# Kernel optimization log

Measured on AMD Instinct MI355X. Metric: run time of the kernel, lower is better.

## Reference

```python
import jax, jax.numpy as jnp
import numpy as np

# Dims (match init_kwargs): d_model=1024, H=16 heads, hd=64, lift=2 -> Nlift=128, top-k t=32
B, T, D = 1, 2048, 1024
H, HD, LIFT, TK = 16, 64, 2, 32
N = LIFT * HD  # 128 lifted dims per head
EPS = 1e-12


def topk_sparsify(x, k):
    """ReLU then keep only the top-k values per last-dim row (rest zeroed).
    Mathematically identical to the torch COO top-k construction: the sparse
    matrix equals the dense matrix with non-top-k entries zeroed."""
    x = jax.nn.relu(x)
    vals, idx = jax.lax.top_k(x, k)              # (..., k)
    n = x.shape[-1]
    flat_idx = idx.reshape(-1, k)
    flat_vals = vals.reshape(-1, k)
    R = flat_idx.shape[0]
    out = jnp.zeros((R, n), dtype=x.dtype)
    out = out.at[jnp.arange(R)[:, None], flat_idx].set(flat_vals)
    return out.reshape(x.shape)


def setup_inputs() -> dict:
    key = jax.random.key(0)
    ks = jax.random.split(key, 6)
    x = jax.random.normal(ks[0], (B, T, D), jnp.float32)
    W_q = jax.random.normal(ks[1], (H * N, D), jnp.float32) * 0.02
    W_k = jax.random.normal(ks[2], (H * N, D), jnp.float32) * 0.02
    W_v = jax.random.normal(ks[3], (H * HD, D), jnp.float32) * 0.02
    W_o = jax.random.normal(ks[4], (D, H * HD), jnp.float32) * 0.02
    sink = jax.random.normal(ks[5], (H, HD), jnp.float32) * 0.02
    log_beta = jnp.zeros((), jnp.float32)
    return {"x": x, "W_q": W_q, "W_k": W_k, "W_v": W_v, "W_o": W_o,
            "sink": sink, "log_beta": log_beta}


def reference(x, W_q, W_k, W_v, W_o, sink, log_beta):
    # Projections (Linear with no bias: x @ W.T)
    q = (x @ W_q.T).reshape(B, T, H, N)
    k = (x @ W_k.T).reshape(B, T, H, N)
    v = (x @ W_v.T).reshape(B, T, H, HD)

    # ReLU + top-k sparsification of lifted Q/K rows
    qs = topk_sparsify(q, TK).transpose(0, 2, 1, 3)  # (B,H,T,N)
    kk = topk_sparsify(k, TK).transpose(0, 2, 1, 3)  # (B,H,T,N)

    # A = Qs @ Ks^T per (batch, head) block; spspmm only produces same-block
    # entries, so the per-head batched matmul is the exact dense equivalent.
    A = jnp.einsum('bhin,bhjn->bhij', qs, kk)        # (B,H,T,T), all >= 0

    # Causal filter: keep j <= i
    causal = jnp.tril(jnp.ones((T, T), dtype=bool))
    A = jnp.where(causal, A, jnp.zeros((), A.dtype))

    # p=1 normalization with learned sink mass beta
    denom = A.sum(-1)                                # (B,H,T)
    beta = jnp.exp(log_beta)
    denom_ws = denom + beta
    A = A / jnp.maximum(denom_ws, EPS)[..., None]

    vh = v.transpose(0, 2, 1, 3)                     # (B,H,T,HD)
    Y = jnp.einsum('bhij,bhjd->bhid', A, vh)         # (B,H,T,HD)
    Y = Y + (beta / denom_ws)[..., None] * sink[None, :, None, :]

    Y = Y.transpose(0, 2, 1, 3).reshape(B, T, H * HD)
    return Y @ W_o.T
```

## Files before the change

### kernel.cpp

```cpp
#include <hip/hip_runtime.h>

typedef __attribute__((ext_vector_type(8))) short bf8v;
typedef __attribute__((ext_vector_type(4))) float f4v;
typedef unsigned short u16;
typedef unsigned int   u32;
#define AS1 __attribute__((address_space(1)))
#define AS3 __attribute__((address_space(3)))

__device__ inline u16 f2b(float f){
  u32 u = __builtin_bit_cast(u32, f);
  u += 0x7fffu + ((u >> 16) & 1u);
  return (u16)(u >> 16);
}

__global__ __launch_bounds__(256) void conv_all(const float* __restrict__ x,  const float* __restrict__ wq,
                                                const float* __restrict__ wk, const float* __restrict__ wv,
                                                const float* __restrict__ wo,
                                                u16* xb, u16* wqb, u16* wkb, u16* wvb, u16* wob){
  int i = blockIdx.x * 256 + threadIdx.x;
  const float* src; u16* dst; int off;
  if      (i <  524288){ src = x;  dst = xb;  off = i; }
  else if (i < 1048576){ src = wq; dst = wqb; off = i -  524288; }
  else if (i < 1572864){ src = wk; dst = wkb; off = i - 1048576; }
  else if (i < 1835008){ src = wv; dst = wvb; off = i - 1572864; }
  else                 { src = wo; dst = wob; off = i - 1835008; }
  float4 v = ((const float4*)src)[off];
  uint2 r;
  r.x = (u32)f2b(v.x) | ((u32)f2b(v.y) << 16);
  r.y = (u32)f2b(v.z) | ((u32)f2b(v.w) << 16);
  ((uint2*)dst)[off] = r;
}

template<int NFR>
__device__ __forceinline__ void gemm_core(const u16* __restrict__ A, const u16* __restrict__ B,
                                          int K, int m0, int n0, u16* lds, f4v (&acc)[4][NFR]){
  const int tid = threadIdx.x;
  const int l = tid & 63, w = tid >> 6;
  const int wrow = (w >> 1) * 64, wcol = (w & 1) * (NFR * 16);
  constexpr int SB = 8192 + NFR * 2048;
  #pragma unroll
  for (int a = 0; a < 4; a++)
    #pragma unroll
    for (int b = 0; b < NFR; b++) acc[a][b] = (f4v)0.0f;

  const int crow = l >> 3;
  const int ksrc = ((l & 7) ^ crow) * 8;

  auto stage = [&](int k0, int buf){
    const u16* Ab = A + (size_t)m0 * K + k0;
    const u16* Bb = B + (size_t)n0 * K + k0;
    u16* At = lds + buf * SB;
    u16* Bt = At + 8192;
    #pragma unroll
    for (int c = 0; c < 4; c++){
      int chunk = w * 4 + c;
      int row = chunk * 8 + crow;
      __builtin_amdgcn_global_load_lds((const AS1 void*)(Ab + (size_t)row * K + ksrc),
                                       (AS3 void*)(At + chunk * 512), 16, 0, 0);
    }
    if constexpr (NFR == 4){
      #pragma unroll
      for (int c = 0; c < 4; c++){
        int chunk = w * 4 + c;
        int row = chunk * 8 + crow;
        __builtin_amdgcn_global_load_lds((const AS1 void*)(Bb + (size_t)row * K + ksrc),
                                         (AS3 void*)(Bt + chunk * 512), 16, 0, 0);
      }
    } else {
      #pragma unroll
      for (int c = 0; c < 2; c++){
        int chunk = w * 2 + c;
        int row = chunk * 8 + crow;
        __builtin_amdgcn_global_load_lds((const AS1 void*)(Bb + (size_t)row * K + ksrc),
                                         (AS3 void*)(Bt + chunk * 512), 16, 0, 0);
      }
    }
  };

  stage(0, 0);
  __syncthreads();
  int buf = 0;
  for (int k0 = 0; k0 < K; k0 += 64){
    if (k0 + 64 < K) stage(k0 + 64, buf ^ 1);
    const u16* At = lds + buf * SB;
    const u16* Bt = At + 8192;
    #pragma unroll
    for (int kk = 0; kk < 2; kk++){
      bf8v af[4], bfr[NFR];
      #pragma unroll
      for (int mr = 0; mr < 4; mr++){
        int row = wrow + mr * 16 + (l & 15);
        af[mr] = *(const bf8v*)(At + row * 64 + (((kk * 32 + (l >> 4) * 8)) ^ ((row & 7) * 8)));
      }
      #pragma unroll
      for (int nc = 0; nc < NFR; nc++){
        int row = wcol + nc * 16 + (l & 15);
        bfr[nc] = *(const bf8v*)(Bt + row * 64 + (((kk * 32 + (l >> 4) * 8)) ^ ((row & 7) * 8)));
      }
      #pragma unroll
      for (int mr = 0; mr < 4; mr++)
        #pragma unroll
        for (int nc = 0; nc < NFR; nc++)
          acc[mr][nc] = __builtin_amdgcn_mfma_f32_16x16x32_bf16(af[mr], bfr[nc], acc[mr][nc], 0, 0, 0);
    }
    __syncthreads();
    buf ^= 1;
  }
}

__global__ __launch_bounds__(256) void qkv_gemm(const u16* __restrict__ xb,
                                                const u16* __restrict__ wqb, const u16* __restrict__ wkb,
                                                const u16* __restrict__ wvb,
                                                u16* qsb, u16* ksb, u16* vtb){
  __shared__ u16 lds[32768];
  int b = (blockIdx.x & 7) * 80 + (blockIdx.x >> 3);
  const u16* Bp; int which;
  if (b < 256)      { Bp = wqb; which = 0; }
  else if (b < 512) { Bp = wkb; which = 1; b -= 256; }
  else              { Bp = wvb; which = 2; b -= 512; }
  int sh = (which == 2) ? 3 : 4;
  int m0 = (b >> sh) * 128, n0 = (b & ((1 << sh) - 1)) * 128;

  f4v acc[4][4];
  gemm_core<4>(xb, Bp, 1024, m0, n0, lds, acc);

  const int l = threadIdx.x & 63, w = threadIdx.x >> 6;
  const int wrow = (w >> 1) * 64, wcol = (w & 1) * 64;
  if (which < 2){
    u16* Sc = lds;
    #pragma unroll
    for (int mr = 0; mr < 4; mr++)
      #pragma unroll
      for (int nc = 0; nc < 4; nc++)
        #pragma unroll
        for (int rr = 0; rr < 4; rr++){
          int row = wrow + mr * 16 + (l >> 4) * 4 + rr;
          int col = wcol + nc * 16 + (l & 15);
          float v = acc[mr][nc][rr];
          Sc[row * 132 + col] = (v > 0.f) ? f2b(v) : (u16)0;
        }
    __syncthreads();
    u16* dst = which ? ksb : qsb;
    const int h = n0 >> 7;
    for (int r2 = 0; r2 < 32; ++r2){
      int r = w * 32 + r2;
      u32 pair = *(const u32*)(Sc + r * 132 + l * 2);
      u32 u0 = pair & 0xFFFFu, u1 = pair >> 16;
      u32 pre = 0;
      for (int bb = 14; bb >= 0; --bb){
        u32 cand = pre | (1u << bb);
        int c = __builtin_popcountll(__ballot(u0 >= cand)) + __builtin_popcountll(__ballot(u1 >= cand));
        if (c >= 32) pre = cand;
      }
      u32 o0 = (u0 >= pre) ? u0 : 0u;
      u32 o1 = (u1 >= pre) ? u1 : 0u;
      ((u32*)(dst + ((size_t)h * 2048 + m0 + r) * 128))[l] = o0 | (o1 << 16);
    }
  } else {
    #pragma unroll
    for (int mr = 0; mr < 4; mr++)
      #pragma unroll
      for (int nc = 0; nc < 4; nc++){
        int gcol = n0 + wcol + nc * 16 + (l & 15);
        int t0 = m0 + wrow + mr * 16 + (l >> 4) * 4;
        uint2 pk;
        pk.x = (u32)f2b(acc[mr][nc][0]) | ((u32)f2b(acc[mr][nc][1]) << 16);
        pk.y = (u32)f2b(acc[mr][nc][2]) | ((u32)f2b(acc[mr][nc][3]) << 16);
        *(uint2*)(vtb + (size_t)gcol * 2048 + t0) = pk;
      }
  }
}

__global__ __launch_bounds__(256) void o_gemm(const u16* __restrict__ yb, const u16* __restrict__ wob,
                                              float* out){
  __shared__ u16 lds[24576];
  int b = (blockIdx.x & 7) * 32 + (blockIdx.x >> 3);
  int m0 = (b >> 4) * 128, n0 = (b & 15) * 64;
  f4v acc[4][2];
  gemm_core<2>(yb, wob, 1024, m0, n0, lds, acc);
  const int l = threadIdx.x & 63, w = threadIdx.x >> 6;
  const int wrow = (w >> 1) * 64, wcol = (w & 1) * 32;
  #pragma unroll
  for (int mr = 0; mr < 4; mr++)
    #pragma unroll
    for (int nc = 0; nc < 2; nc++)
      #pragma unroll
      for (int rr = 0; rr < 4; rr++){
        int row = m0 + wrow + mr * 16 + (l >> 4) * 4 + rr;
        int col = n0 + wcol + nc * 16 + (l & 15);
        out[(size_t)row * 1024 + col] = acc[mr][nc][rr];
      }
}

__global__ __launch_bounds__(512) void attn3(const u16* __restrict__ qs, const u16* __restrict__ ks,
                                             const u16* __restrict__ vt, const float* __restrict__ sink,
                                             const float* __restrict__ logbeta, u16* __restrict__ yout,
                                             float* __restrict__ Yp, float* __restrict__ Dp){
  __shared__ u16 Kt[2][8192];
  __shared__ u16 Vt[2][4096];
  __shared__ u16 St[8][16 * 72];
  const int tid = threadIdx.x, l = tid & 63, w = tid >> 6;
  const int b = blockIdx.x;
  const int slot = b >> 3;
  const int h = (b & 7) + 8 * (slot / 40);
  const int u = slot % 40;
  int it, chunk, nch;
  if (u < 4)       { it = u; chunk = 0; nch = 1; }
  else if (u < 12) { it = 4 + ((u - 4) >> 1);  chunk = (u - 4) & 1;  nch = 2; }
  else if (u < 24) { it = 8 + (u - 12) / 3;    chunk = (u - 12) % 3; nch = 3; }
  else             { it = 12 + ((u - 24) >> 2); chunk = (u - 24) & 3; nch = 4; }
  const int tiles = 2 * it + 2;
  const int jt0 = (tiles * chunk) / nch;
  const int jt1 = (tiles * (chunk + 1)) / nch;
  const int qrow0 = it * 128 + w * 16;
  const float beta = expf(logbeta[0]);

  bf8v qfr[4];
  {
    int trow = qrow0 + (l & 15);
    const u16* qrow = qs + ((size_t)h * 2048 + trow) * 128 + (l >> 4) * 8;
    #pragma unroll
    for (int kk = 0; kk < 4; kk++) qfr[kk] = *(const bf8v*)(qrow + kk * 32);
  }

  f4v accY[4];
  #pragma unroll
  for (int c = 0; c < 4; c++) accY[c] = (f4v)0.0f;
  float dsum[4] = {0.f, 0.f, 0.f, 0.f};

  const u16* kroot = ks + (size_t)h * 2048 * 128;
  const u16* vroot = vt + (size_t)h * 64 * 2048;

  auto stage = [&](int jt, int buf){
    const u16* kbase = kroot + (size_t)jt * 64 * 128;
    #pragma unroll
    for (int i = 0; i < 2; i++){
      int g = i * 512 + tid;
      int r = g >> 4, c = g & 15;
      __builtin_amdgcn_global_load_lds((const AS1 void*)(kbase + r * 128 + (c ^ (r & 7)) * 8),
                                       (AS3 void*)(&Kt[buf][(i * 512 + w * 64) * 8]), 16, 0, 0);
    }
    {
      int d = tid >> 3, c = tid & 7;
      __builtin_amdgcn_global_load_lds((const AS1 void*)(vroot + (size_t)d * 2048 + jt * 64 + (c ^ (d & 7)) * 8),
                                       (AS3 void*)(&Vt[buf][w * 512]), 16, 0, 0);
    }
  };

  stage(jt0, 0);
  __syncthreads();
  int buf = 0;
  for (int jt = jt0; jt < jt1; ++jt){
    if (jt + 1 < jt1) stage(jt + 1, buf ^ 1);

    if (jt * 64 <= qrow0 + 15){
      f4v accS[4];
      #pragma unroll
      for (int c = 0; c < 4; c++) accS[c] = (f4v)0.0f;
      __builtin_amdgcn_s_setprio(1);
      #pragma unroll
      for (int c = 0; c < 4; c++){
        int r = c * 16 + (l & 15);
        #pragma unroll
        for (int kk = 0; kk < 4; kk++){
          int ch = kk * 4 + (l >> 4);
          bf8v kfr = *(const bf8v*)(&Kt[buf][r * 128 + ((ch ^ (r & 7)) * 8)]);
          accS[c] = __builtin_amdgcn_mfma_f32_16x16x32_bf16(qfr[kk], kfr, accS[c], 0, 0, 0);
        }
      }
      __builtin_amdgcn_s_setprio(0);
      if (jt * 64 + 63 > qrow0){
        #pragma unroll
        for (int c = 0; c < 4; c++)
          #pragma unroll
          for (int rr = 0; rr < 4; rr++){
            int i = qrow0 + (l >> 4) * 4 + rr;
            int j = jt * 64 + c * 16 + (l & 15);
            if (j > i) accS[c][rr] = 0.f;
          }
      }
      #pragma unroll
      for (int c = 0; c < 4; c++)
        #pragma unroll
        for (int rr = 0; rr < 4; rr++){
          dsum[rr] += accS[c][rr];
          St[w][((l >> 4) * 4 + rr) * 72 + c * 16 + (l & 15)] = f2b(accS[c][rr]);
        }
      __builtin_amdgcn_s_setprio(1);
      #pragma unroll
      for (int k2 = 0; k2 < 2; k2++){
        bf8v afr = *(const bf8v*)(&St[w][(l & 15) * 72 + k2 * 32 + (l >> 4) * 8]);
        #pragma unroll
        for (int c = 0; c < 4; c++){
          int d = c * 16 + (l & 15);
          int ch = k2 * 4 + (l >> 4);
          bf8v vfr = *(const bf8v*)(&Vt[buf][d * 64 + ((ch ^ (d & 7)) * 8)]);
          accY[c] = __builtin_amdgcn_mfma_f32_16x16x32_bf16(afr, vfr, accY[c], 0, 0, 0);
        }
      }
      __builtin_amdgcn_s_setprio(0);
    }
    __syncthreads();
    buf ^= 1;
  }

  #pragma unroll
  for (int rr = 0; rr < 4; rr++){
    float s = dsum[rr];
    s += __shfl_xor(s, 1, 64);
    s += __shfl_xor(s, 2, 64);
    s += __shfl_xor(s, 4, 64);
    s += __shfl_xor(s, 8, 64);
    dsum[rr] = s;
  }

  if (nch == 1){
    #pragma unroll
    for (int c = 0; c < 4; c++){
      float sv = sink[h * 64 + c * 16 + (l & 15)];
      #pragma unroll
      for (int rr = 0; rr < 4; rr++){
        float den = dsum[rr] + beta;
        float inv = 1.0f / fmaxf(den, 1e-12f);
        float y = (accY[c][rr] + beta * sv) * inv;
        int row = qrow0 + (l >> 4) * 4 + rr;
        yout[(size_t)row * 1024 + h * 64 + c * 16 + (l & 15)] = f2b(y);
      }
    }
  } else {
    float* yp = Yp + ((size_t)h * 40 + u) * 8192;
    #pragma unroll
    for (int c = 0; c < 4; c++)
      #pragma unroll
      for (int rr = 0; rr < 4; rr++){
        int rowib = w * 16 + (l >> 4) * 4 + rr;
        yp[rowib * 64 + c * 16 + (l & 15)] = accY[c][rr];
      }
    if ((l & 15) == 0){
      #pragma unroll
      for (int rr = 0; rr < 4; rr++)
        Dp[((size_t)h * 40 + u) * 128 + w * 16 + (l >> 4) * 4 + rr] = dsum[rr];
    }
  }
}

__global__ __launch_bounds__(256) void attn_reduce(const float* __restrict__ Yp, const float* __restrict__ Dp,
                                                   const float* __restrict__ sink, const float* __restrict__ logbeta,
                                                   u16* __restrict__ yout){
  int blk = blockIdx.x;
  int h = blk / 12, it = 4 + blk % 12;
  int nch = it / 4 + 1;
  int u0 = (it < 8) ? 4 + (it - 4) * 2 : (it < 12) ? 12 + (it - 8) * 3 : 24 + (it - 12) * 4;
  float beta = expf(logbeta[0]);
  __shared__ float inv_s[128];
  int t = threadIdx.x;
  if (t < 128){
    float s = 0.f;
    for (int c = 0; c < nch; c++) s += Dp[((size_t)h * 40 + u0 + c) * 128 + t];
    inv_s[t] = 1.0f / fmaxf(s + beta, 1e-12f);
  }
  __syncthreads();
  const float* base = Yp + ((size_t)h * 40 + u0) * 8192;
  #pragma unroll
  for (int e = 0; e < 32; e++){
    int idx = e * 256 + t;
    float acc = 0.f;
    for (int c = 0; c < nch; c++) acc += base[c * 8192 + idx];
    int row = idx >> 6, col = idx & 63;
    float y = (acc + beta * sink[h * 64 + col]) * inv_s[row];
    yout[(size_t)(it * 128 + row) * 1024 + h * 64 + col] = f2b(y);
  }
}

extern "C" void kernel_launch(void* const* d_in, const int* in_sizes, int n_in,
                              void* d_out, int out_size, void* d_ws, size_t ws_size,
                              hipStream_t stream){
  const float* x    = (const float*)d_in[0];
  const float* Wq   = (const float*)d_in[1];
  const float* Wk   = (const float*)d_in[2];
  const float* Wv   = (const float*)d_in[3];
  const float* Wo   = (const float*)d_in[4];
  const float* sink = (const float*)d_in[5];
  const float* logb = (const float*)d_in[6];

  char* ws = (char*)d_ws;
  u16*   xb  = (u16*)(ws + 0);
  u16*   wqb = (u16*)(ws + 4194304);
  u16*   wkb = (u16*)(ws + 8388608);
  u16*   wvb = (u16*)(ws + 12582912);
  u16*   wob = (u16*)(ws + 14680064);
  float* Yp  = (float*)(ws + 16777216);
  float* Dp  = (float*)(ws + 37748736);
  u16*   qsb = (u16*)(ws + 50331648);
  u16*   ksb = (u16*)(ws + 58720256);
  u16*   vtb = (u16*)(ws + 67108864);
  u16*   yb  = (u16*)(ws + 71303168);

  conv_all<<<8192, 256, 0, stream>>>(x, Wq, Wk, Wv, Wo, xb, wqb, wkb, wvb, wob);
  qkv_gemm<<<640, 256, 0, stream>>>(xb, wqb, wkb, wvb, qsb, ksb, vtb);
  attn3<<<640, 512, 0, stream>>>(qsb, ksb, vtb, sink, logb, yb, Yp, Dp);
  attn_reduce<<<192, 256, 0, stream>>>(Yp, Dp, sink, logb, yb);
  o_gemm<<<256, 256, 0, stream>>>(yb, wob, (float*)d_out);
}
```

Measured before the change: 149.6 us.

## Split top-k sparsification out of QKV GEMM epilogue into separate kernel

The QKV GEMM now writes raw bf16 Q/K projections to a workspace buffer. A new topk2 kernel then applies ReLU and the bitwise threshold search for the top-32 per row, handling four rows per wave so the serial ballot loop gains instruction-level parallelism. This removes the long serial epilogue from the GEMM blocks, but it adds a kernel launch and an extra global write and read of the full Q/K tensors. The workspace region used for the partial Y buffers is reused for these intermediates.

```diff
diff --git a/kernel.cpp b/kernel.cpp
--- a/kernel.cpp
+++ b/kernel.cpp
@@ -111,7 +111,7 @@
 __global__ __launch_bounds__(256) void qkv_gemm(const u16* __restrict__ xb,
                                                 const u16* __restrict__ wqb, const u16* __restrict__ wkb,
                                                 const u16* __restrict__ wvb,
-                                                u16* qsb, u16* ksb, u16* vtb){
+                                                u16* qf, u16* kf, u16* vtb){
   __shared__ u16 lds[32768];
   int b = (blockIdx.x & 7) * 80 + (blockIdx.x >> 3);
   const u16* Bp; int which;
@@ -127,35 +127,17 @@
   const int l = threadIdx.x & 63, w = threadIdx.x >> 6;
   const int wrow = (w >> 1) * 64, wcol = (w & 1) * 64;
   if (which < 2){
-    u16* Sc = lds;
+    u16* C = which ? kf : qf;
     #pragma unroll
     for (int mr = 0; mr < 4; mr++)
       #pragma unroll
       for (int nc = 0; nc < 4; nc++)
         #pragma unroll
         for (int rr = 0; rr < 4; rr++){
-          int row = wrow + mr * 16 + (l >> 4) * 4 + rr;
-          int col = wcol + nc * 16 + (l & 15);
-          float v = acc[mr][nc][rr];
-          Sc[row * 132 + col] = (v > 0.f) ? f2b(v) : (u16)0;
+          int row = m0 + wrow + mr * 16 + (l >> 4) * 4 + rr;
+          int col = n0 + wcol + nc * 16 + (l & 15);
+          C[(size_t)row * 2048 + col] = f2b(acc[mr][nc][rr]);
         }
-    __syncthreads();
-    u16* dst = which ? ksb : qsb;
-    const int h = n0 >> 7;
-    for (int r2 = 0; r2 < 32; ++r2){
-      int r = w * 32 + r2;
-      u32 pair = *(const u32*)(Sc + r * 132 + l * 2);
-      u32 u0 = pair & 0xFFFFu, u1 = pair >> 16;
-      u32 pre = 0;
-      for (int bb = 14; bb >= 0; --bb){
-        u32 cand = pre | (1u << bb);
-        int c = __builtin_popcountll(__ballot(u0 >= cand)) + __builtin_popcountll(__ballot(u1 >= cand));
-        if (c >= 32) pre = cand;
-      }
-      u32 o0 = (u0 >= pre) ? u0 : 0u;
-      u32 o1 = (u1 >= pre) ? u1 : 0u;
-      ((u32*)(dst + ((size_t)h * 2048 + m0 + r) * 128))[l] = o0 | (o1 << 16);
-    }
   } else {
     #pragma unroll
     for (int mr = 0; mr < 4; mr++)
@@ -190,6 +172,41 @@
         int col = n0 + wcol + nc * 16 + (l & 15);
         out[(size_t)row * 1024 + col] = acc[mr][nc][rr];
       }
+}
+
+__global__ __launch_bounds__(256) void topk2(const u16* __restrict__ qf, const u16* __restrict__ kf,
+                                             u16* __restrict__ qsb, u16* __restrict__ ksb){
+  int w = threadIdx.x >> 6, l = threadIdx.x & 63;
+  int b = blockIdx.x;
+  const u16* src; u16* dst;
+  if (b < 2048){ src = qf; dst = qsb; } else { src = kf; dst = ksb; b -= 2048; }
+  int base = b * 16 + w * 4;
+  u32 u0[4], u1[4], pre[4];
+  int tt[4], hh[4];
+  #pragma unroll
+  for (int j = 0; j < 4; j++){
+    int r = base + j;
+    tt[j] = r >> 4; hh[j] = r & 15;
+    u32 pair = ((const u32*)(src + (size_t)tt[j] * 2048 + hh[j] * 128))[l];
+    u0[j] = pair & 0xFFFFu; u1[j] = pair >> 16;
+    if (u0[j] & 0x8000u) u0[j] = 0;
+    if (u1[j] & 0x8000u) u1[j] = 0;
+    pre[j] = 0;
+  }
+  for (int bb = 14; bb >= 0; --bb){
+    #pragma unroll
+    for (int j = 0; j < 4; j++){
+      u32 cand = pre[j] | (1u << bb);
+      int c = __builtin_popcountll(__ballot(u0[j] >= cand)) + __builtin_popcountll(__ballot(u1[j] >= cand));
+      if (c >= 32) pre[j] = cand;
+    }
+  }
+  #pragma unroll
+  for (int j = 0; j < 4; j++){
+    u32 o0 = (u0[j] >= pre[j]) ? u0[j] : 0u;
+    u32 o1 = (u1[j] >= pre[j]) ? u1[j] : 0u;
+    ((u32*)(dst + ((size_t)hh[j] * 2048 + tt[j]) * 128))[l] = o0 | (o1 << 16);
+  }
 }
 
 __global__ __launch_bounds__(512) void attn3(const u16* __restrict__ qs, const u16* __restrict__ ks,
@@ -389,15 +406,18 @@
   u16*   wkb = (u16*)(ws + 8388608);
   u16*   wvb = (u16*)(ws + 12582912);
   u16*   wob = (u16*)(ws + 14680064);
-  float* Yp  = (float*)(ws + 16777216);
-  float* Dp  = (float*)(ws + 37748736);
+  u16*   qf  = (u16*)(ws + 16777216);
+  u16*   kf  = (u16*)(ws + 33554432);
   u16*   qsb = (u16*)(ws + 50331648);
   u16*   ksb = (u16*)(ws + 58720256);
   u16*   vtb = (u16*)(ws + 67108864);
   u16*   yb  = (u16*)(ws + 71303168);
+  float* Yp  = (float*)(ws + 16777216);
+  float* Dp  = (float*)(ws + 37748736);
 
   conv_all<<<8192, 256, 0, stream>>>(x, Wq, Wk, Wv, Wo, xb, wqb, wkb, wvb, wob);
-  qkv_gemm<<<640, 256, 0, stream>>>(xb, wqb, wkb, wvb, qsb, ksb, vtb);
+  qkv_gemm<<<640, 256, 0, stream>>>(xb, wqb, wkb, wvb, qf, kf, vtb);
+  topk2<<<4096, 256, 0, stream>>>(qf, kf, qsb, ksb);
   attn3<<<640, 512, 0, stream>>>(qsb, ksb, vtb, sink, logb, yb, Yp, Dp);
   attn_reduce<<<192, 256, 0, stream>>>(Yp, Dp, sink, logb, yb);
   o_gemm<<<256, 256, 0, stream>>>(yb, wob, (float*)d_out);
```

New measurement: 140.7 us. 5.9% less time.
